# Optimization experiments

Hardware: AMD Instinct MI355X
Metric: run time of the kernel (lower is better)

Reference implementation:

```python
import jax, jax.numpy as jnp
import numpy as np

NUM_HEADS = 16
B, S, D = 2, 2048, 1024


def setup_inputs() -> dict:
    key = jax.random.key(0)
    ks = jax.random.split(key, 6)
    return {
        "q": jax.random.normal(ks[0], (B, S, D), dtype=jnp.float32),
        "k": jax.random.normal(ks[1], (B, S, D), dtype=jnp.float32),
        "v": jax.random.normal(ks[2], (B, S, D), dtype=jnp.float32),
        "wq": jax.random.normal(ks[3], (D, D), dtype=jnp.float32) * (1.0 / np.sqrt(D)),
        "wk": jax.random.normal(ks[4], (D, D), dtype=jnp.float32) * (1.0 / np.sqrt(D)),
        "wv": jax.random.normal(ks[5], (D, D), dtype=jnp.float32) * (1.0 / np.sqrt(D)),
    }


def reference(q, k, v, wq, wk, wv):
    b, s, d = q.shape
    h = NUM_HEADS
    hd = d // h

    def proj(x, w):
        # torch Linear (no bias): x @ w.T ; chunk(dim=2) == reshape to heads
        return (x @ w.T).reshape(b, s, h, hd).transpose(0, 2, 1, 3)  # [b,h,s,hd]

    qh, kh, vh = proj(q, wq), proj(k, wk), proj(v, wv)
    scale = 1.0 / jnp.sqrt(jnp.asarray(hd, q.dtype))
    scores = jnp.einsum("bhqd,bhkd->bhqk", qh, kh) * scale  # [b,h,s,s]
    # faithful to torch: .tril() zeroes (not -inf) the upper triangle pre-softmax
    mask = jnp.tril(jnp.ones((s, s), dtype=bool))
    scores = jnp.where(mask, scores, jnp.asarray(0.0, scores.dtype))
    attn = jax.nn.softmax(scores, axis=-1)
    out = jnp.einsum("bhqk,bhkd->bhqd", attn, vh)  # [b,h,s,hd]
    return out.transpose(0, 2, 1, 3).reshape(b, s, d)
```

## Files before the change

kernel.cpp:

```cpp
#include <hip/hip_runtime.h>
#include <math.h>

#define B_  2
#define S_  2048
#define D_  1024
#define H_  16
#define HD_ 64
#define NT_ (S_/64)
#define C2_ (0.125f * 1.44269504088896f)

typedef __attribute__((ext_vector_type(8))) _Float16 f16x8;
typedef __attribute__((ext_vector_type(2))) __fp16 h16x2;
typedef __attribute__((ext_vector_type(4))) float f32x4;
typedef unsigned short u16;
typedef unsigned int   u32;

__device__ inline u16 f2h(float f) {
    union { _Float16 h; u16 u; } c; c.h = (_Float16)f;
    return c.u;
}
__device__ inline u32 pkrtz(float a, float b) {
    union { h16x2 h; u32 u; } c;
    c.h = __builtin_amdgcn_cvt_pkrtz(a, b);
    return c.u;
}

#define GLOAD_LDS16(g, l)                                                    \
    __builtin_amdgcn_global_load_lds(                                        \
        (const __attribute__((address_space(1))) void*)(g),                  \
        (__attribute__((address_space(3))) void*)(l), 16, 0, 0)

__global__ __launch_bounds__(256)
void precast(const float* __restrict__ wq, const float* __restrict__ wk,
             const float* __restrict__ wv, const float* __restrict__ q,
             const float* __restrict__ k,  const float* __restrict__ v,
             u16* __restrict__ Wq, u16* __restrict__ Wk, u16* __restrict__ Wv,
             u16* __restrict__ Xq, u16* __restrict__ Xk, u16* __restrict__ Xv)
{
    const int z = blockIdx.y;
    const size_t n = (z >= 3) ? (size_t)B_ * S_ * D_ : (size_t)D_ * D_;
    const size_t i = ((size_t)blockIdx.x * 256 + threadIdx.x) * 4;
    if (i >= n) return;
    const float* src = (z == 0) ? wq : (z == 1) ? wk : (z == 2) ? wv
                     : (z == 3) ? q  : (z == 4) ? k  : v;
    u16* dst = (z == 0) ? Wq : (z == 1) ? Wk : (z == 2) ? Wv
             : (z == 3) ? Xq : (z == 4) ? Xk : Xv;
    float4 xv = *(const float4*)&src[i];
    *(ushort4*)&dst[i] = make_ushort4(f2h(xv.x), f2h(xv.y), f2h(xv.z), f2h(xv.w));
}

__global__ __launch_bounds__(256)
void proj_all(const u16* __restrict__ Xq, const u16* __restrict__ Xk,
              const u16* __restrict__ Xv, const u16* __restrict__ Wq,
              const u16* __restrict__ Wk, const u16* __restrict__ Wv,
              u16* __restrict__ QP, u16* __restrict__ KP, u16* __restrict__ VT)
{
    const int bid = (int)blockIdx.x;
    const int g   = (bid & 7) * 96 + (bid >> 3);
    const int z   = g >> 8;
    const int rem = g & 255;
    const int ny  = rem >> 3;
    const int nx  = rem & 7;

    const u16* X = (z == 0) ? Xq : (z == 1) ? Xk : Xv;
    const u16* W = (z == 0) ? Wq : (z == 1) ? Wk : Wv;

    __shared__ u16 Xs[128 * 64];
    __shared__ u16 Ws[128 * 64];

    const int tid  = threadIdx.x;
    const int w    = tid >> 6;
    const int lane = tid & 63;
    const int quad = lane >> 4;
    const int lr   = lane & 15;
    const int m0   = ny * 128;
    const int n0   = nx * 128;

    const int srow  = w * 32 + (lane >> 3);
    const int gslot = (lane & 7) ^ ((lane >> 3) & 7);
    const size_t xbase = (size_t)(m0 + srow) * D_ + gslot * 8;
    const size_t wbase = (size_t)(n0 + srow) * D_ + gslot * 8;
    const int ldsoff = w * 2048 + lane * 8;

    f32x4 acc[2][8];
    #pragma unroll
    for (int i = 0; i < 2; ++i)
        #pragma unroll
        for (int j = 0; j < 8; ++j) acc[i][j] = (f32x4){0.f, 0.f, 0.f, 0.f};

    for (int k0 = 0; k0 < D_; k0 += 64) {
        __syncthreads();
        #pragma unroll
        for (int c = 0; c < 4; ++c) {
            GLOAD_LDS16(X + xbase + (size_t)c * 8 * D_ + k0, &Xs[ldsoff + c * 512]);
            GLOAD_LDS16(W + wbase + (size_t)c * 8 * D_ + k0, &Ws[ldsoff + c * 512]);
        }
        __syncthreads();

        #pragma unroll
        for (int ch = 0; ch < 2; ++ch) {
            const int sl = ((ch * 4 + quad) ^ (lr & 7)) * 8;
            f16x8 a[2];
            #pragma unroll
            for (int i = 0; i < 2; ++i)
                a[i] = *(const f16x8*)&Xs[(w * 32 + i * 16 + lr) * 64 + sl];
            #pragma unroll
            for (int j = 0; j < 8; ++j) {
                f16x8 b = *(const f16x8*)&Ws[(j * 16 + lr) * 64 + sl];
                #pragma unroll
                for (int i = 0; i < 2; ++i)
                    acc[i][j] = __builtin_amdgcn_mfma_f32_16x16x32_f16(a[i], b, acc[i][j], 0, 0, 0);
            }
        }
    }

    if (z < 2) {
        u16* P = (z == 0) ? QP : KP;
        const float sc = (z == 0) ? C2_ : 1.0f;
        #pragma unroll
        for (int i = 0; i < 2; ++i)
            #pragma unroll
            for (int j = 0; j < 8; ++j) {
                int n = n0 + j * 16 + lr;
                int h = n >> 6, hd = n & 63;
                #pragma unroll
                for (int r = 0; r < 4; ++r) {
                    int m = m0 + w * 32 + i * 16 + quad * 4 + r;
                    int b = m >> 11, s = m & (S_ - 1);
                    P[(((size_t)b * H_ + h) * S_ + s) * HD_ + hd] = f2h(acc[i][j][r] * sc);
                }
            }
    } else {
        #pragma unroll
        for (int i = 0; i < 2; ++i)
            #pragma unroll
            for (int j = 0; j < 8; ++j) {
                int n  = n0 + j * 16 + lr;
                int h  = n >> 6, vd = n & 63;
                int m  = m0 + w * 32 + i * 16 + quad * 4;
                int b  = m >> 11, s = m & (S_ - 1);
                ushort4 pv = make_ushort4(f2h(acc[i][j][0]), f2h(acc[i][j][1]),
                                          f2h(acc[i][j][2]), f2h(acc[i][j][3]));
                *(ushort4*)&VT[(((size_t)b * H_ + h) * HD_ + vd) * S_ + s] = pv;
            }
    }
}

__global__ __launch_bounds__(64)
void vtilesum_kernel(const u16* __restrict__ VT, float* __restrict__ TS)
{
    const int t = blockIdx.x, bh = blockIdx.y, vd = threadIdx.x;
    const u16* p = VT + ((size_t)bh * HD_ + vd) * S_ + t * 64;
    float acc = 0.f;
    #pragma unroll
    for (int c = 0; c < 8; ++c) {
        f16x8 vv = *(const f16x8*)&p[c * 8];
        #pragma unroll
        for (int j = 0; j < 8; ++j) acc += (float)vv[j];
    }
    TS[((size_t)bh * NT_ + t) * HD_ + vd] = acc;
}

__global__ __launch_bounds__(64)
void vsuffix_kernel(const float* __restrict__ TS, float* __restrict__ SUF)
{
    const int bh = blockIdx.x, c = threadIdx.x;
    float acc = 0.f;
    SUF[((size_t)bh * (NT_ + 1) + NT_) * HD_ + c] = 0.f;
    for (int t = NT_ - 1; t >= 0; --t) {
        acc += TS[((size_t)bh * NT_ + t) * HD_ + c];
        SUF[((size_t)bh * (NT_ + 1) + t) * HD_ + c] = acc;
    }
}

__global__ __launch_bounds__(256)
void attn_mfma(const u16* __restrict__ QP, const u16* __restrict__ KP,
               const u16* __restrict__ VT, const float* __restrict__ SUF,
               float* __restrict__ OUT)
{
    const int bh = blockIdx.x;
    const int tq = NT_ - 1 - (int)blockIdx.y;
    const int b  = bh >> 4, h = bh & 15;

    __shared__ u16 Ks[64][72];
    __shared__ u16 Vth[64][72];
    __shared__ u16 Phi[4][16][72];

    const int tid  = threadIdx.x;
    const int w    = tid >> 6;
    const int lane = tid & 63;
    const int quad = lane >> 4;
    const int lr   = lane & 15;
    const int r    = tid >> 2;
    const int cb   = (tid & 3) * 16;

    const u16* Qb = QP + (size_t)bh * S_ * HD_;
    const u16* Kb = KP + (size_t)bh * S_ * HD_;
    const u16* Vb = VT + (size_t)bh * HD_ * S_;

    const int q0 = tq * 64;

    f16x8 qf[2];
    #pragma unroll
    for (int ch = 0; ch < 2; ++ch)
        qf[ch] = *(const f16x8*)(Qb + (size_t)(q0 + w * 16 + lr) * HD_ +
                                 ch * 32 + quad * 8);

    f32x4 of[4];
    #pragma unroll
    for (int n = 0; n < 4; ++n) of[n] = (f32x4){0.f, 0.f, 0.f, 0.f};
    float l_i = 0.f;

    f16x8 kpre[2], vpre[2];
    #pragma unroll
    for (int c = 0; c < 2; ++c) {
        kpre[c] = *(const f16x8*)(Kb + (size_t)r * HD_ + cb + c * 8);
        vpre[c] = *(const f16x8*)(Vb + (size_t)r * S_ + cb + c * 8);
    }

    for (int t = 0; t <= tq; ++t) {
        const int k0t = t * 64;
        __syncthreads();
        #pragma unroll
        for (int c = 0; c < 2; ++c) {
            *(f16x8*)&Ks[r][cb + c * 8]  = kpre[c];
            *(f16x8*)&Vth[r][cb + c * 8] = vpre[c];
        }
        __syncthreads();
        if (t < tq) {
            const int kn = k0t + 64;
            #pragma unroll
            for (int c = 0; c < 2; ++c) {
                kpre[c] = *(const f16x8*)(Kb + (size_t)(kn + r) * HD_ + cb + c * 8);
                vpre[c] = *(const f16x8*)(Vb + (size_t)r * S_ + kn + cb + c * 8);
            }
        }

        f32x4 sf[4];
        #pragma unroll
        for (int f = 0; f < 4; ++f) sf[f] = (f32x4){0.f, 0.f, 0.f, 0.f};
        #pragma unroll
        for (int ch = 0; ch < 2; ++ch)
            #pragma unroll
            for (int f = 0; f < 4; ++f) {
                f16x8 ak = *(const f16x8*)&Ks[f * 16 + lr][ch * 32 + quad * 8];
                sf[f] = __builtin_amdgcn_mfma_f32_16x16x32_f16(ak, qf[ch], sf[f], 0, 0, 0);
            }

        if (t == tq) {
            const int ig = q0 + w * 16 + lr;
            #pragma unroll
            for (int f = 0; f < 4; ++f)
                #pragma unroll
                for (int i = 0; i < 4; ++i) {
                    int jg = k0t + f * 16 + quad * 4 + i;
                    sf[f][i] = (jg <= ig) ? sf[f][i] : 0.f;
                }
        }

        float ps = 0.f;
        #pragma unroll
        for (int f = 0; f < 4; ++f)
            #pragma unroll
            for (int i = 0; i < 4; ++i) {
                float p = exp2f(sf[f][i]);
                sf[f][i] = p;
                ps += p;
            }
        ps += __shfl_xor(ps, 16);
        ps += __shfl_xor(ps, 32);
        l_i += ps;

        #pragma unroll
        for (int f = 0; f < 4; ++f) {
            *(u32*)&Phi[w][lr][f * 16 + quad * 4]     = pkrtz(sf[f][0], sf[f][1]);
            *(u32*)&Phi[w][lr][f * 16 + quad * 4 + 2] = pkrtz(sf[f][2], sf[f][3]);
        }

        #pragma unroll
        for (int ch = 0; ch < 2; ++ch) {
            f16x8 pb = *(const f16x8*)&Phi[w][lr][ch * 32 + quad * 8];
            #pragma unroll
            for (int n = 0; n < 4; ++n) {
                f16x8 av = *(const f16x8*)&Vth[n * 16 + lr][ch * 32 + quad * 8];
                of[n] = __builtin_amdgcn_mfma_f32_16x16x32_f16(av, pb, of[n], 0, 0, 0);
            }
        }
    }

    const int cnt = S_ - (q0 + 64);
    const float* suf = SUF + ((size_t)bh * (NT_ + 1) + (tq + 1)) * HD_;
    float inv = 1.0f / (l_i + (float)cnt);
    const int srow = q0 + w * 16 + lr;
    #pragma unroll
    for (int n = 0; n < 4; ++n) {
        float4 sv = *(const float4*)&suf[n * 16 + quad * 4];
        float4 ov;
        ov.x = (of[n][0] + sv.x) * inv;
        ov.y = (of[n][1] + sv.y) * inv;
        ov.z = (of[n][2] + sv.z) * inv;
        ov.w = (of[n][3] + sv.w) * inv;
        *(float4*)&OUT[((size_t)b * S_ + srow) * D_ + h * HD_ + n * 16 + quad * 4] = ov;
    }
}

extern "C" void kernel_launch(void* const* d_in, const int* in_sizes, int n_in,
                              void* d_out, int out_size, void* d_ws, size_t ws_size,
                              hipStream_t stream)
{
    (void)in_sizes; (void)n_in; (void)out_size; (void)ws_size;
    const float* q  = (const float*)d_in[0];
    const float* k  = (const float*)d_in[1];
    const float* v  = (const float*)d_in[2];
    const float* wq = (const float*)d_in[3];
    const float* wk = (const float*)d_in[4];
    const float* wv = (const float*)d_in[5];
    float* out = (float*)d_out;

    const size_t PROJ = (size_t)B_ * H_ * S_ * HD_;
    const size_t WSZ  = (size_t)D_ * D_;
    u16* QP = (u16*)d_ws;
    u16* KP = QP + PROJ;
    u16* VT = KP + PROJ;
    u16* Xq = VT + PROJ;
    u16* Xk = Xq + PROJ;
    u16* Xv = Xk + PROJ;
    u16* Wq = Xv + PROJ;
    u16* Wk = Wq + WSZ;
    u16* Wv = Wk + WSZ;
    float* TS  = (float*)(Wv + WSZ);
    float* SUF = TS + (size_t)B_ * H_ * NT_ * HD_;

    precast<<<dim3(PROJ / 1024, 6), 256, 0, stream>>>(
        wq, wk, wv, q, k, v, Wq, Wk, Wv, Xq, Xk, Xv);
    proj_all<<<dim3(3 * (D_ / 128) * ((B_ * S_) / 128)), 256, 0, stream>>>(
        Xq, Xk, Xv, Wq, Wk, Wv, QP, KP, VT);
    vtilesum_kernel<<<dim3(NT_, B_ * H_), 64, 0, stream>>>(VT, TS);
    vsuffix_kernel<<<B_ * H_, 64, 0, stream>>>(TS, SUF);
    attn_mfma<<<dim3(B_ * H_, NT_), 256, 0, stream>>>(QP, KP, VT, SUF, out);
}
```

Before: 194.6 us.

## Enlarge projection GEMM tile to 256x256 with double-buffered LDS prefetch

```diff
diff --git a/kernel.cpp b/kernel.cpp
--- a/kernel.cpp
+++ b/kernel.cpp
@@ -49,32 +49,34 @@
     *(ushort4*)&dst[i] = make_ushort4(f2h(xv.x), f2h(xv.y), f2h(xv.z), f2h(xv.w));
 }
 
-__global__ __launch_bounds__(256)
+__global__ __launch_bounds__(512, 2)
 void proj_all(const u16* __restrict__ Xq, const u16* __restrict__ Xk,
               const u16* __restrict__ Xv, const u16* __restrict__ Wq,
               const u16* __restrict__ Wk, const u16* __restrict__ Wv,
               u16* __restrict__ QP, u16* __restrict__ KP, u16* __restrict__ VT)
 {
     const int bid = (int)blockIdx.x;
-    const int g   = (bid & 7) * 96 + (bid >> 3);
-    const int z   = g >> 8;
-    const int rem = g & 255;
-    const int ny  = rem >> 3;
-    const int nx  = rem & 7;
+    const int g   = (bid & 7) * 24 + (bid >> 3);
+    const int z   = g >> 6;
+    const int rem = g & 63;
+    const int my  = rem >> 2;
+    const int nx  = rem & 3;
 
     const u16* X = (z == 0) ? Xq : (z == 1) ? Xk : Xv;
     const u16* W = (z == 0) ? Wq : (z == 1) ? Wk : Wv;
 
-    __shared__ u16 Xs[128 * 64];
-    __shared__ u16 Ws[128 * 64];
+    __shared__ u16 Xs[2][256 * 64];
+    __shared__ u16 Ws[2][256 * 64];
 
     const int tid  = threadIdx.x;
     const int w    = tid >> 6;
     const int lane = tid & 63;
     const int quad = lane >> 4;
     const int lr   = lane & 15;
-    const int m0   = ny * 128;
-    const int n0   = nx * 128;
+    const int wm   = w >> 2;
+    const int wn   = w & 3;
+    const int m0   = my * 256;
+    const int n0   = nx * 256;
 
     const int srow  = w * 32 + (lane >> 3);
     const int gslot = (lane & 7) ^ ((lane >> 3) & 7);
@@ -82,65 +84,115 @@
     const size_t wbase = (size_t)(n0 + srow) * D_ + gslot * 8;
     const int ldsoff = w * 2048 + lane * 8;
 
-    f32x4 acc[2][8];
-    #pragma unroll
-    for (int i = 0; i < 2; ++i)
-        #pragma unroll
-        for (int j = 0; j < 8; ++j) acc[i][j] = (f32x4){0.f, 0.f, 0.f, 0.f};
-
-    for (int k0 = 0; k0 < D_; k0 += 64) {
-        __syncthreads();
-        #pragma unroll
-        for (int c = 0; c < 4; ++c) {
-            GLOAD_LDS16(X + xbase + (size_t)c * 8 * D_ + k0, &Xs[ldsoff + c * 512]);
-            GLOAD_LDS16(W + wbase + (size_t)c * 8 * D_ + k0, &Ws[ldsoff + c * 512]);
-        }
-        __syncthreads();
-
-        #pragma unroll
-        for (int ch = 0; ch < 2; ++ch) {
-            const int sl = ((ch * 4 + quad) ^ (lr & 7)) * 8;
-            f16x8 a[2];
-            #pragma unroll
-            for (int i = 0; i < 2; ++i)
-                a[i] = *(const f16x8*)&Xs[(w * 32 + i * 16 + lr) * 64 + sl];
-            #pragma unroll
-            for (int j = 0; j < 8; ++j) {
-                f16x8 b = *(const f16x8*)&Ws[(j * 16 + lr) * 64 + sl];
+    f32x4 acc[8][4];
+    #pragma unroll
+    for (int i = 0; i < 8; ++i)
+        #pragma unroll
+        for (int j = 0; j < 4; ++j) acc[i][j] = (f32x4){0.f, 0.f, 0.f, 0.f};
+
+    #pragma unroll
+    for (int c = 0; c < 4; ++c) {
+        GLOAD_LDS16(X + xbase + (size_t)c * 8 * D_, &Xs[0][ldsoff + c * 512]);
+        GLOAD_LDS16(W + wbase + (size_t)c * 8 * D_, &Ws[0][ldsoff + c * 512]);
+    }
+
+    for (int t = 0; t < 16; ++t) {
+        const int cur = t & 1;
+        if (t < 15) {
+            const size_t ko = (size_t)(t + 1) * 64;
+            #pragma unroll
+            for (int c = 0; c < 4; ++c) {
+                GLOAD_LDS16(X + xbase + (size_t)c * 8 * D_ + ko,
+                            &Xs[cur ^ 1][ldsoff + c * 512]);
+                GLOAD_LDS16(W + wbase + (size_t)c * 8 * D_ + ko,
+                            &Ws[cur ^ 1][ldsoff + c * 512]);
+            }
+            asm volatile("s_waitcnt vmcnt(8)" ::: "memory");
+        } else {
+            asm volatile("s_waitcnt vmcnt(0)" ::: "memory");
+        }
+        __builtin_amdgcn_s_barrier();
+
+        f16x8 bf[4][2], af[4][2];
+        #pragma unroll
+        for (int fn = 0; fn < 4; ++fn) {
+            const int row = wn * 64 + fn * 16 + lr;
+            #pragma unroll
+            for (int kk = 0; kk < 2; ++kk)
+                bf[fn][kk] = *(const f16x8*)
+                    &Ws[cur][row * 64 + (((kk * 4 + quad) ^ (lr & 7)) << 3)];
+        }
+        #pragma unroll
+        for (int fm = 0; fm < 4; ++fm) {
+            const int row = wm * 128 + fm * 16 + lr;
+            #pragma unroll
+            for (int kk = 0; kk < 2; ++kk)
+                af[fm][kk] = *(const f16x8*)
+                    &Xs[cur][row * 64 + (((kk * 4 + quad) ^ (lr & 7)) << 3)];
+        }
+        __builtin_amdgcn_s_barrier();
+        __builtin_amdgcn_s_setprio(1);
+        #pragma unroll
+        for (int fm = 0; fm < 4; ++fm)
+            #pragma unroll
+            for (int fn = 0; fn < 4; ++fn)
                 #pragma unroll
-                for (int i = 0; i < 2; ++i)
-                    acc[i][j] = __builtin_amdgcn_mfma_f32_16x16x32_f16(a[i], b, acc[i][j], 0, 0, 0);
-            }
-        }
+                for (int kk = 0; kk < 2; ++kk)
+                    acc[fm][fn] = __builtin_amdgcn_mfma_f32_16x16x32_f16(
+                        af[fm][kk], bf[fn][kk], acc[fm][fn], 0, 0, 0);
+        __builtin_amdgcn_s_setprio(0);
+        __builtin_amdgcn_s_barrier();
+
+        #pragma unroll
+        for (int fm = 0; fm < 4; ++fm) {
+            const int row = wm * 128 + 64 + fm * 16 + lr;
+            #pragma unroll
+            for (int kk = 0; kk < 2; ++kk)
+                af[fm][kk] = *(const f16x8*)
+                    &Xs[cur][row * 64 + (((kk * 4 + quad) ^ (lr & 7)) << 3)];
+        }
+        __builtin_amdgcn_s_barrier();
+        __builtin_amdgcn_s_setprio(1);
+        #pragma unroll
+        for (int fm = 0; fm < 4; ++fm)
+            #pragma unroll
+            for (int fn = 0; fn < 4; ++fn)
+                #pragma unroll
+                for (int kk = 0; kk < 2; ++kk)
+                    acc[4 + fm][fn] = __builtin_amdgcn_mfma_f32_16x16x32_f16(
+                        af[fm][kk], bf[fn][kk], acc[4 + fm][fn], 0, 0, 0);
+        __builtin_amdgcn_s_setprio(0);
+        __builtin_amdgcn_s_barrier();
     }
 
     if (z < 2) {
         u16* P = (z == 0) ? QP : KP;
         const float sc = (z == 0) ? C2_ : 1.0f;
         #pragma unroll
-        for (int i = 0; i < 2; ++i)
-            #pragma unroll
-            for (int j = 0; j < 8; ++j) {
-                int n = n0 + j * 16 + lr;
+        for (int fm = 0; fm < 8; ++fm)
+            #pragma unroll
+            for (int fn = 0; fn < 4; ++fn) {
+                int n = n0 + wn * 64 + fn * 16 + lr;
                 int h = n >> 6, hd = n & 63;
                 #pragma unroll
                 for (int r = 0; r < 4; ++r) {
-                    int m = m0 + w * 32 + i * 16 + quad * 4 + r;
+                    int m = m0 + wm * 128 + fm * 16 + quad * 4 + r;
                     int b = m >> 11, s = m & (S_ - 1);
-                    P[(((size_t)b * H_ + h) * S_ + s) * HD_ + hd] = f2h(acc[i][j][r] * sc);
+                    P[(((size_t)b * H_ + h) * S_ + s) * HD_ + hd] =
+                        f2h(acc[fm][fn][r] * sc);
                 }
             }
     } else {
         #pragma unroll
-        for (int i = 0; i < 2; ++i)
-            #pragma unroll
-            for (int j = 0; j < 8; ++j) {
-                int n  = n0 + j * 16 + lr;
+        for (int fm = 0; fm < 8; ++fm)
+            #pragma unroll
+            for (int fn = 0; fn < 4; ++fn) {
+                int n  = n0 + wn * 64 + fn * 16 + lr;
                 int h  = n >> 6, vd = n & 63;
-                int m  = m0 + w * 32 + i * 16 + quad * 4;
+                int m  = m0 + wm * 128 + fm * 16 + quad * 4;
                 int b  = m >> 11, s = m & (S_ - 1);
-                ushort4 pv = make_ushort4(f2h(acc[i][j][0]), f2h(acc[i][j][1]),
-                                          f2h(acc[i][j][2]), f2h(acc[i][j][3]));
+                ushort4 pv = make_ushort4(f2h(acc[fm][fn][0]), f2h(acc[fm][fn][1]),
+                                          f2h(acc[fm][fn][2]), f2h(acc[fm][fn][3]));
                 *(ushort4*)&VT[(((size_t)b * H_ + h) * HD_ + vd) * S_ + s] = pv;
             }
     }
@@ -333,7 +385,7 @@
 
     precast<<<dim3(PROJ / 1024, 6), 256, 0, stream>>>(
         wq, wk, wv, q, k, v, Wq, Wk, Wv, Xq, Xk, Xv);
-    proj_all<<<dim3(3 * (D_ / 128) * ((B_ * S_) / 128)), 256, 0, stream>>>(
+    proj_all<<<dim3(3 * (D_ / 256) * ((B_ * S_) / 256)), 512, 0, stream>>>(
         Xq, Xk, Xv, Wq, Wk, Wv, QP, KP, VT);
     vtilesum_kernel<<<dim3(NT_, B_ * H_), 64, 0, stream>>>(VT, TS);
     vsuffix_kernel<<<B_ * H_, 64, 0, stream>>>(TS, SUF);
```

Result: no change. 194.4 us (-0.1%).
